# Kernel tuning notes

Measured on AMD Instinct MI355X. Metric: run time of the kernel, lower is better.

The kernel has to match this reference:

```python
import jax, jax.numpy as jnp
import numpy as np

SLOPE = 0.1  # supar MLP uses LeakyReLU(0.1)

def _mlp(x, W, b):
    return jax.nn.leaky_relu(x @ W + b, negative_slope=SLOPE)

def _triaffine(x, y, z, W):
    # supar Triaffine with n_out=1: s[b,z,x,y] = sum_{i,k,j} x[b,x,i] W[i,k,j] y[b,y,j] z[b,z,k]
    w = jnp.einsum('bzk,ikj->bzij', z, W)          # [b, n, d, d]
    return jnp.einsum('bxi,bzij,byj->bzxy', x, w, y)  # [b, n, n, n]

def _triu_sym(s):
    # s.triu() + s.triu(1).transpose(-1, -2) over last two dims
    return jnp.triu(s) + jnp.swapaxes(jnp.triu(s, 1), -1, -2)

def setup_inputs() -> dict:
    key = jax.random.key(0)
    B, N, D_IN, D = 2, 128, 1024, 150
    ks = jax.random.split(key, 16)
    sc_in = 1.0 / np.sqrt(D_IN)
    sc_tri = float(D) ** -1.5  # keeps triaffine outputs O(1)
    def nrm(k, shape, sc):
        return jax.random.normal(k, shape, jnp.float32) * sc
    return {
        'x':   jax.random.normal(ks[0], (B, N, D_IN), jnp.float32),
        'W_sh': nrm(ks[1], (D_IN, D), sc_in), 'b_sh': jnp.zeros((D,), jnp.float32),
        'W_st': nrm(ks[2], (D_IN, D), sc_in), 'b_st': jnp.zeros((D,), jnp.float32),
        'W_p':  nrm(ks[3], (D_IN, D), sc_in), 'b_p':  jnp.zeros((D,), jnp.float32),
        'T_pt':    nrm(ks[4], (D, D, D), sc_tri),
        'T_ph':    nrm(ks[5], (D, D, D), sc_tri),
        'T_phsib': nrm(ks[6], (D, D, D), sc_tri),
        'T_ptsib': nrm(ks[7], (D, D, D), sc_tri),
        'T_phcop': nrm(ks[8], (D, D, D), sc_tri),
        'T_ptcop': nrm(ks[9], (D, D, D), sc_tri),
    }

def reference(x, W_sh, b_sh, W_st, b_st, W_p, b_p,
              T_pt, T_ph, T_phsib, T_ptsib, T_phcop, T_ptcop):
    # eval mode: dropout is identity; ind_prd=False so p2 == p (shared MLP)
    sh = _mlp(x, W_sh, b_sh)
    st = _mlp(x, W_st, b_st)
    p = _mlp(x, W_p, b_p)
    p2 = p
    # span scores: [b, p, sh_idx, st_idx]
    span_pst = _triu_sym(_triaffine(sh, st, p2, T_pt))
    span_psh = _triaffine(sh, st, p, T_ph)
    # sibling scores: [b, p, h, h'] / [b, p, t, t']
    ph_sib = _triu_sym(_triaffine(sh, sh, p, T_phsib))
    pt_sib = _triu_sym(_triaffine(st, st, p2, T_ptsib))
    # co-parent scores: triaffine gives [b, h, p, p'], permute(0,2,3,1) -> [b, p, p', h]
    ph_cop = jnp.transpose(_triu_sym(_triaffine(p, p, sh, T_phcop)), (0, 2, 3, 1))
    pt_cop = jnp.transpose(_triu_sym(_triaffine(p2, p2, st, T_ptcop)), (0, 2, 3, 1))
    return (span_psh, span_pst, ph_sib, pt_sib, ph_cop, pt_cop)
```

## Files before the change

### kernel.cpp

```cpp
#include <hip/hip_runtime.h>


#define DD    150
#define KP    160
#define OUTBLK 4194304
#define NWZ   24064
#define TTG   3840000
#define WZG   (256*NWZ)
#define HROW  (256*160)

__device__ __forceinline__ unsigned short f2u(float f) {
  unsigned x = __float_as_uint(f);
  x += 0x7FFFu + ((x >> 16) & 1u);
  return (unsigned short)(x >> 16);
}

typedef __attribute__((ext_vector_type(8))) short frag8;
typedef __attribute__((ext_vector_type(4))) float facc4;
typedef __attribute__((ext_vector_type(4))) unsigned uint4v;

__constant__ int c_zsel[6] = {2, 2, 2, 2, 0, 1};
__constant__ int c_xsel[6] = {0, 0, 0, 1, 2, 2};
__constant__ int c_ysel[6] = {1, 1, 0, 1, 2, 2};

__global__ __launch_bounds__(256) void mlp_partial(
    const float* __restrict__ x,
    const float* __restrict__ W0, const float* __restrict__ W1, const float* __restrict__ W2,
    float* __restrict__ P)
{
  int m = blockIdx.x, bt = blockIdx.y, ks = blockIdx.z;
  const float* W = (m == 0) ? W0 : (m == 1) ? W1 : W2;
  int bn0 = bt * 32, k0 = ks * 128;
  __shared__ float xs[32][132];
  int tid = threadIdx.x;
  for (int e = 0; e < 4; ++e) {
    int l = e * 256 + tid;
    int row = l >> 5, c4 = l & 31;
    float4 v = *(const float4*)&x[(bn0 + row) * 1024 + k0 + c4 * 4];
    xs[row][c4 * 4 + 0] = v.x; xs[row][c4 * 4 + 1] = v.y;
    xs[row][c4 * 4 + 2] = v.z; xs[row][c4 * 4 + 3] = v.w;
  }
  __syncthreads();
  int tj = tid & 15, tt = tid >> 4, r = tt * 2;
  int dd[10];
  #pragma unroll
  for (int u = 0; u < 10; ++u) { int d = tj + 16 * u; dd[u] = d < 150 ? d : 149; }
  float a0[10], a1[10];
  #pragma unroll
  for (int u = 0; u < 10; ++u) { a0[u] = 0.f; a1[u] = 0.f; }
  for (int k = 0; k < 128; ++k) {
    float xa = xs[r][k], xb = xs[r + 1][k];
    const float* wr = W + (long long)(k0 + k) * 150;
    #pragma unroll
    for (int u = 0; u < 10; ++u) {
      float w = wr[dd[u]];
      a0[u] += xa * w; a1[u] += xb * w;
    }
  }
  float* Pb = P + (long long)(m * 8 + ks) * 256 * 160;
  #pragma unroll
  for (int u = 0; u < 10; ++u) {
    int d = tj + 16 * u;
    Pb[(bn0 + r) * 160 + d]     = a0[u];
    Pb[(bn0 + r + 1) * 160 + d] = a1[u];
  }
}

__global__ __launch_bounds__(256) void mlp_reduce(
    const float* __restrict__ P,
    const float* __restrict__ B0, const float* __restrict__ B1, const float* __restrict__ B2,
    unsigned short* __restrict__ H)
{
  int o = blockIdx.x * 256 + threadIdx.x;
  int d = o % 160;
  int bn = (o / 160) & 255;
  int m = o / (160 * 256);
  float v = 0.f;
  if (d < 150) {
    const float* Bv = (m == 0) ? B0 : (m == 1) ? B1 : B2;
    v = Bv[d];
    #pragma unroll
    for (int ks = 0; ks < 8; ++ks)
      v += P[((long long)(m * 8 + ks) * 256 + bn) * 160 + d];
    v = v > 0.f ? v : 0.1f * v;
  }
  H[o] = f2u(v);
}

struct TPtrs { const float* t[6]; };
__global__ __launch_bounds__(256) void tt_kernel(TPtrs tp, unsigned short* __restrict__ TT3)
{
  int i = blockIdx.x;
  int ky = blockIdx.y % 5, jy = blockIdx.y / 5;
  int k0 = ky * 32, j0 = jy * 32;
  int g = blockIdx.z;
  const float* T = tp.t[g];
  unsigned short* TT = TT3 + (long long)g * TTG;
  __shared__ float tl[32][33];
  int tid = threadIdx.x;
  #pragma unroll
  for (int e = 0; e < 4; ++e) {
    int l = e * 256 + tid;
    int r = l >> 5, c = l & 31;
    float v = 0.f;
    if (i < 150 && k0 + r < 150 && j0 + c < 150)
      v = T[i * 22500 + (k0 + r) * 150 + (j0 + c)];
    tl[r][c] = v;
  }
  __syncthreads();
  #pragma unroll
  for (int e = 0; e < 4; ++e) {
    int l = e * 256 + tid;
    int rr = l >> 5, cc = l & 31;
    if (j0 + rr < 150)
      TT[(long long)((j0 + rr) * 160 + i) * 160 + k0 + cc] = f2u(tl[cc][rr]);
  }
}

__global__ __launch_bounds__(256) void wz_gemm(
    const unsigned short* __restrict__ Hb, const unsigned short* __restrict__ TT3,
    unsigned short* __restrict__ wz3)
{
  constexpr int LR = 72;
  __shared__ unsigned short lA[128 * LR];
  __shared__ unsigned short lB[128 * LR];
  int g = blockIdx.z, tid = threadIdx.x;
  const unsigned short* Ab = Hb + c_zsel[g] * HROW + blockIdx.y * 128 * 160;
  const unsigned short* Bb = TT3 + (long long)g * TTG;
  int n0 = blockIdx.x * 128;
  int wave = tid >> 6, lane = tid & 63;
  int l15 = lane & 15, lq = lane >> 4;
  int mw = (wave & 1) * 64, nw = (wave >> 1) * 64;
  facc4 acc[4][4];
  #pragma unroll
  for (int i = 0; i < 4; ++i)
    #pragma unroll
    for (int j = 0; j < 4; ++j) acc[i][j] = (facc4){0.f, 0.f, 0.f, 0.f};
  for (int ch = 0; ch < 3; ++ch) {
    int k0 = ch << 6;
    int sh = (ch == 2) ? 2 : 3, upr = 1 << sh;
    for (int u = tid; u < 128 * upr; u += 256) {
      int row = u >> sh, off = (u & (upr - 1)) << 3;
      *(uint4*)&lA[row * LR + off] = *(const uint4*)&Ab[row * 160 + k0 + off];
    }
    for (int u = tid; u < 128 * upr; u += 256) {
      int row = u >> sh, off = (u & (upr - 1)) << 3;
      int gn = n0 + row;
      uint4 v; v.x = 0u; v.y = 0u; v.z = 0u; v.w = 0u;
      if (gn < 24000) v = *(const uint4*)&Bb[(long long)gn * 160 + k0 + off];
      *(uint4*)&lB[row * LR + off] = v;
    }
    __syncthreads();
    int nks = (ch == 2) ? 1 : 2;
    for (int ks = 0; ks < nks; ++ks) {
      int ko = (ks << 5) + (lq << 3);
      frag8 af[4], bfr[4];
      #pragma unroll
      for (int i = 0; i < 4; ++i) af[i] = *(const frag8*)&lA[(mw + i * 16 + l15) * LR + ko];
      #pragma unroll
      for (int j = 0; j < 4; ++j) bfr[j] = *(const frag8*)&lB[(nw + j * 16 + l15) * LR + ko];
      #pragma unroll
      for (int i = 0; i < 4; ++i)
        #pragma unroll
        for (int j = 0; j < 4; ++j)
          acc[i][j] = __builtin_amdgcn_mfma_f32_16x16x32_bf16(af[i], bfr[j], acc[i][j], 0, 0, 0);
    }
    __syncthreads();
  }
  unsigned short* C = wz3 + (long long)g * WZG;
  int mb = blockIdx.y * 128 + mw;
  #pragma unroll
  for (int i = 0; i < 4; ++i)
    #pragma unroll
    for (int r = 0; r < 4; ++r) {
      int m = mb + i * 16 + lq * 4 + r;
      #pragma unroll
      for (int j = 0; j < 4; ++j)
        C[(long long)m * NWZ + n0 + nw + j * 16 + l15] = f2u(acc[i][j][r]);
    }
}

struct SPtrs { float* p[6]; };
__global__ __launch_bounds__(256, 3) void tmps_gemm(
    const unsigned short* __restrict__ Hb, const unsigned short* __restrict__ wz3,
    SPtrs sp)
{
  __shared__ union {
    struct { unsigned short X[128 * 72]; unsigned short W[160 * 72]; } p1;
    unsigned short Y[128 * 168];
    float sq[64 * 129];
  } sm;

  int z = blockIdx.x, tid = threadIdx.x;
  int g = z >> 8, bz = z & 255, b = bz >> 7;
  const unsigned short* Ab = Hb + c_xsel[g] * HROW + b * 128 * 160;
  const unsigned short* Wb = wz3 + (long long)g * WZG + (long long)bz * NWZ;
  int wave = tid >> 6, lane = tid & 63;
  int l15 = lane & 15, lq = lane >> 4;
  int X0 = wave * 32;

  facc4 accT[10][2];
  #pragma unroll
  for (int jt = 0; jt < 10; ++jt)
    #pragma unroll
    for (int xt = 0; xt < 2; ++xt) accT[jt][xt] = (facc4){0.f, 0.f, 0.f, 0.f};
  for (int ch = 0; ch < 3; ++ch) {
    int k0 = ch << 6;
    int sh = (ch == 2) ? 2 : 3, upr = 1 << sh;
    for (int u = tid; u < 128 * upr; u += 256) {
      int row = u >> sh, off = (u & (upr - 1)) << 3;
      *(uint4*)&sm.p1.X[row * 72 + off] = *(const uint4*)&Ab[row * 160 + k0 + off];
    }
    for (int u = tid; u < 160 * upr; u += 256) {
      int row = u >> sh, off = (u & (upr - 1)) << 3;
      uint4 v; v.x = 0u; v.y = 0u; v.z = 0u; v.w = 0u;
      if (row < 150) v = *(const uint4*)&Wb[row * 160 + k0 + off];
      *(uint4*)&sm.p1.W[row * 72 + off] = v;
    }
    __syncthreads();
    int nks = (ch == 2) ? 1 : 2;
    for (int ks = 0; ks < nks; ++ks) {
      int ko = (ks << 5) + (lq << 3);
      frag8 bx0 = *(const frag8*)&sm.p1.X[(X0 + l15) * 72 + ko];
      frag8 bx1 = *(const frag8*)&sm.p1.X[(X0 + 16 + l15) * 72 + ko];
      #pragma unroll
      for (int jt = 0; jt < 10; ++jt) {
        frag8 aw = *(const frag8*)&sm.p1.W[(jt * 16 + l15) * 72 + ko];
        accT[jt][0] = __builtin_amdgcn_mfma_f32_16x16x32_bf16(aw, bx0, accT[jt][0], 0, 0, 0);
        accT[jt][1] = __builtin_amdgcn_mfma_f32_16x16x32_bf16(aw, bx1, accT[jt][1], 0, 0, 0);
      }
    }
    __syncthreads();
  }

  frag8 pA[2][5];
  {
    int s0 = ((lq & 1) << 5) + l15;
    int s2 = s0 + 16;
    bool lo = lq < 2;
    #pragma unroll
    for (int kb = 0; kb < 5; ++kb)
      #pragma unroll
      for (int xt = 0; xt < 2; ++xt) {
        unsigned w0l = (unsigned)f2u(accT[2 * kb][xt][0]) |
                       ((unsigned)f2u(accT[2 * kb][xt][1]) << 16);
        unsigned w1l = (unsigned)f2u(accT[2 * kb][xt][2]) |
                       ((unsigned)f2u(accT[2 * kb][xt][3]) << 16);
        unsigned w0h = (unsigned)f2u(accT[2 * kb + 1][xt][0]) |
                       ((unsigned)f2u(accT[2 * kb + 1][xt][1]) << 16);
        unsigned w1h = (unsigned)f2u(accT[2 * kb + 1][xt][2]) |
                       ((unsigned)f2u(accT[2 * kb + 1][xt][3]) << 16);
        unsigned a0 = __shfl(w0l, s0), b0 = __shfl(w0h, s0);
        unsigned a1 = __shfl(w1l, s0), b1 = __shfl(w1h, s0);
        unsigned a2 = __shfl(w0l, s2), b2 = __shfl(w0h, s2);
        unsigned a3 = __shfl(w1l, s2), b3 = __shfl(w1h, s2);
        uint4v uv;
        uv.x = lo ? a0 : b0;
        uv.y = lo ? a1 : b1;
        uv.z = lo ? a2 : b2;
        uv.w = lo ? a3 : b3;
        pA[xt][kb] = __builtin_bit_cast(frag8, uv);
      }
  }

  const unsigned short* Yb = Hb + c_ysel[g] * HROW + b * 128 * 160;
  {
    int y = tid & 127, part = tid >> 7;
    #pragma unroll
    for (int p = 0; p < 10; ++p) {
      int off = part * 80 + p * 8;
      *(uint4*)&sm.Y[y * 168 + off] = *(const uint4*)&Yb[y * 160 + off];
    }
  }
  __syncthreads();

  facc4 acc2[2][8];
  #pragma unroll
  for (int xt = 0; xt < 2; ++xt)
    #pragma unroll
    for (int yt = 0; yt < 8; ++yt) acc2[xt][yt] = (facc4){0.f, 0.f, 0.f, 0.f};
  #pragma unroll
  for (int ks = 0; ks < 5; ++ks) {
    int ko = (ks << 5) + (lq << 3);
    #pragma unroll
    for (int yt = 0; yt < 8; ++yt) {
      frag8 by = *(const frag8*)&sm.Y[(yt * 16 + l15) * 168 + ko];
      acc2[0][yt] = __builtin_amdgcn_mfma_f32_16x16x32_bf16(pA[0][ks], by, acc2[0][yt], 0, 0, 0);
      acc2[1][yt] = __builtin_amdgcn_mfma_f32_16x16x32_bf16(pA[1][ks], by, acc2[1][yt], 0, 0, 0);
    }
  }

  float* C = sp.p[g] + (long long)bz * 16384;
  if (g == 0) {
    #pragma unroll
    for (int xt = 0; xt < 2; ++xt)
      #pragma unroll
      for (int r = 0; r < 4; ++r) {
        int x = X0 + xt * 16 + lq * 4 + r;
        #pragma unroll
        for (int yt = 0; yt < 8; ++yt)
          C[x * 128 + yt * 16 + l15] = acc2[xt][yt][r];
      }
  } else if (g >= 4) {
    #pragma unroll
    for (int xt = 0; xt < 2; ++xt)
      #pragma unroll
      for (int r = 0; r < 4; ++r) {
        int x = X0 + xt * 16 + lq * 4 + r;
        #pragma unroll
        for (int yt = 0; yt < 8; ++yt) {
          int y = yt * 16 + l15;
          if (x <= y) C[x * 128 + y] = acc2[xt][yt][r];
        }
      }
  } else {
    #pragma unroll
    for (int xt = 0; xt < 2; ++xt)
      #pragma unroll
      for (int r = 0; r < 4; ++r) {
        int x = X0 + xt * 16 + lq * 4 + r;
        #pragma unroll
        for (int yt = 0; yt < 8; ++yt) {
          int y = yt * 16 + l15;
          if (y >= x) C[x * 128 + y] = acc2[xt][yt][r];
        }
      }
    __syncthreads();
    if (wave < 2) {
      #pragma unroll
      for (int xt = 0; xt < 2; ++xt)
        #pragma unroll
        for (int r = 0; r < 4; ++r) {
          int x = X0 + xt * 16 + lq * 4 + r;
          #pragma unroll
          for (int yt = 0; yt < 8; ++yt)
            sm.sq[x * 129 + yt * 16 + l15] = acc2[xt][yt][r];
        }
    }
    __syncthreads();
    for (int it = 0; it < 32; ++it) {
      int x = X0 + it;
      int y = lane;
      if (y < 64 && y < x) C[x * 128 + y] = sm.sq[y * 129 + x];
    }
    __syncthreads();
    if (wave >= 2) {
      #pragma unroll
      for (int xt = 0; xt < 2; ++xt)
        #pragma unroll
        for (int r = 0; r < 4; ++r) {
          int x = X0 + xt * 16 + lq * 4 + r;
          #pragma unroll
          for (int yt = 0; yt < 8; ++yt)
            sm.sq[(x - 64) * 129 + yt * 16 + l15] = acc2[xt][yt][r];
        }
    }
    __syncthreads();
    for (int it = 0; it < 16; ++it) {
      int x = 64 + wave * 16 + it;
      int y = 64 + lane;
      if (y < x) C[x * 128 + y] = sm.sq[(y - 64) * 129 + x];
    }
  }
}

__global__ __launch_bounds__(256) void cop_kernel(
    const float* __restrict__ ss, float* __restrict__ out)
{
  int w0 = blockIdx.x << 5;
  int z0 = blockIdx.y << 5;
  int g  = blockIdx.z >> 1, b = blockIdx.z & 1;
  const float* sg = ss + (long long)g * OUTBLK;
  float* outp = out + (long long)(4 + g) * OUTBLK;
  __shared__ float tl[32][33];
  int tid = threadIdx.x;
  #pragma unroll
  for (int e = 0; e < 4; ++e) {
    int l = e * 256 + tid;
    int r = l >> 5, c = l & 31;
    int w = w0 + c;
    int xx = w >> 7, yy = w & 127;
    int sx = xx < yy ? xx : yy;
    int sy = xx < yy ? yy : xx;
    tl[r][c] = sg[(((b << 7) + z0 + r) << 14) + (sx << 7) + sy];
  }
  __syncthreads();
  #pragma unroll
  for (int e = 0; e < 4; ++e) {
    int l = e * 256 + tid;
    int rr = l >> 5, cc = l & 31;
    outp[(b << 21) + ((w0 + rr) << 7) + z0 + cc] = tl[cc][rr];
  }
}

extern "C" void kernel_launch(void* const* d_in, const int* in_sizes, int n_in,
                              void* d_out, int out_size, void* d_ws, size_t ws_size,
                              hipStream_t stream)
{
  const float* x   = (const float*)d_in[0];
  const float* Wsh = (const float*)d_in[1];
  const float* bsh = (const float*)d_in[2];
  const float* Wst = (const float*)d_in[3];
  const float* bst = (const float*)d_in[4];
  const float* Wp  = (const float*)d_in[5];
  const float* bp  = (const float*)d_in[6];
  TPtrs tp;
  tp.t[0] = (const float*)d_in[8];
  tp.t[1] = (const float*)d_in[7];
  tp.t[2] = (const float*)d_in[9];
  tp.t[3] = (const float*)d_in[10];
  tp.t[4] = (const float*)d_in[11];
  tp.t[5] = (const float*)d_in[12];
  float* out = (float*)d_out;
  char* wsb = (char*)d_ws;

  unsigned short* Hb   = (unsigned short*)(wsb);
  unsigned short* TT3  = (unsigned short*)(wsb + 245760);
  unsigned short* wz3  = (unsigned short*)(wsb + 46325760);
  float* P  = (float*)wz3;
  float* ss = (float*)TT3;

  SPtrs sp;
  sp.p[0] = out + 0LL * OUTBLK;
  sp.p[1] = out + 1LL * OUTBLK;
  sp.p[2] = out + 2LL * OUTBLK;
  sp.p[3] = out + 3LL * OUTBLK;
  sp.p[4] = ss;
  sp.p[5] = ss + OUTBLK;

  mlp_partial<<<dim3(3, 8, 8),    256, 0, stream>>>(x, Wsh, Wst, Wp, P);
  mlp_reduce <<<dim3(480),        256, 0, stream>>>(P, bsh, bst, bp, Hb);
  tt_kernel  <<<dim3(160, 25, 6), 256, 0, stream>>>(tp, TT3);
  wz_gemm    <<<dim3(188, 2, 6),  256, 0, stream>>>(Hb, TT3, wz3);
  tmps_gemm  <<<dim3(1536),       256, 0, stream>>>(Hb, wz3, sp);
  cop_kernel <<<dim3(512, 4, 4),  256, 0, stream>>>(ss, out);
}
```

Measured before the change: 370.1 us.

## Stream X/Y fragments from global in tmps_gemm and move symmetrize to separate kernel

The tmps_gemm kernel stops staging the X and Y operands in shared memory and loads MFMA fragments directly from global memory, keeping only the W tile in LDS. The second GEMM is split into two halves to reduce accumulator registers, and the launch bound is raised to 4 blocks per CU. The in-kernel transpose-based lower-triangle fill for groups 1-3 is replaced by a new sym_fill kernel that mirrors the upper triangle using 32x32 shared-memory tiles. The aim is lower LDS use and fewer barriers for higher occupancy, at the cost of uncoalesced global fragment loads and an extra launch that rereads the outputs.

```diff
diff --git a/kernel.cpp b/kernel.cpp
--- a/kernel.cpp
+++ b/kernel.cpp
@@ -22,6 +22,8 @@
 __constant__ int c_zsel[6] = {2, 2, 2, 2, 0, 1};
 __constant__ int c_xsel[6] = {0, 0, 0, 1, 2, 2};
 __constant__ int c_ysel[6] = {1, 1, 0, 1, 2, 2};
+__constant__ int c_tx[10] = {0, 1, 1, 2, 2, 2, 3, 3, 3, 3};
+__constant__ int c_ty[10] = {0, 0, 1, 0, 1, 2, 0, 1, 2, 3};
 
 __global__ __launch_bounds__(256) void mlp_partial(
     const float* __restrict__ x,
@@ -181,15 +183,11 @@
 }
 
 struct SPtrs { float* p[6]; };
-__global__ __launch_bounds__(256, 3) void tmps_gemm(
+__global__ __launch_bounds__(256, 4) void tmps_gemm(
     const unsigned short* __restrict__ Hb, const unsigned short* __restrict__ wz3,
     SPtrs sp)
 {
-  __shared__ union {
-    struct { unsigned short X[128 * 72]; unsigned short W[160 * 72]; } p1;
-    unsigned short Y[128 * 168];
-    float sq[64 * 129];
-  } sm;
+  __shared__ unsigned short Wsm[160 * 72];
 
   int z = blockIdx.x, tid = threadIdx.x;
   int g = z >> 8, bz = z & 255, b = bz >> 7;
@@ -199,6 +197,9 @@
   int l15 = lane & 15, lq = lane >> 4;
   int X0 = wave * 32;
 
+  const unsigned short* Xr0 = Ab + (X0 + l15) * 160;
+  const unsigned short* Xr1 = Ab + (X0 + 16 + l15) * 160;
+
   facc4 accT[10][2];
   #pragma unroll
   for (int jt = 0; jt < 10; ++jt)
@@ -207,25 +208,21 @@
   for (int ch = 0; ch < 3; ++ch) {
     int k0 = ch << 6;
     int sh = (ch == 2) ? 2 : 3, upr = 1 << sh;
-    for (int u = tid; u < 128 * upr; u += 256) {
-      int row = u >> sh, off = (u & (upr - 1)) << 3;
-      *(uint4*)&sm.p1.X[row * 72 + off] = *(const uint4*)&Ab[row * 160 + k0 + off];
-    }
     for (int u = tid; u < 160 * upr; u += 256) {
       int row = u >> sh, off = (u & (upr - 1)) << 3;
       uint4 v; v.x = 0u; v.y = 0u; v.z = 0u; v.w = 0u;
       if (row < 150) v = *(const uint4*)&Wb[row * 160 + k0 + off];
-      *(uint4*)&sm.p1.W[row * 72 + off] = v;
+      *(uint4*)&Wsm[row * 72 + off] = v;
     }
     __syncthreads();
     int nks = (ch == 2) ? 1 : 2;
     for (int ks = 0; ks < nks; ++ks) {
       int ko = (ks << 5) + (lq << 3);
-      frag8 bx0 = *(const frag8*)&sm.p1.X[(X0 + l15) * 72 + ko];
-      frag8 bx1 = *(const frag8*)&sm.p1.X[(X0 + 16 + l15) * 72 + ko];
+      frag8 bx0 = *(const frag8*)&Xr0[k0 + ko];
+      frag8 bx1 = *(const frag8*)&Xr1[k0 + ko];
       #pragma unroll
       for (int jt = 0; jt < 10; ++jt) {
-        frag8 aw = *(const frag8*)&sm.p1.W[(jt * 16 + l15) * 72 + ko];
+        frag8 aw = *(const frag8*)&Wsm[(jt * 16 + l15) * 72 + ko];
         accT[jt][0] = __builtin_amdgcn_mfma_f32_16x16x32_bf16(aw, bx0, accT[jt][0], 0, 0, 0);
         accT[jt][1] = __builtin_amdgcn_mfma_f32_16x16x32_bf16(aw, bx1, accT[jt][1], 0, 0, 0);
       }
@@ -264,103 +261,59 @@
   }
 
   const unsigned short* Yb = Hb + c_ysel[g] * HROW + b * 128 * 160;
-  {
-    int y = tid & 127, part = tid >> 7;
-    #pragma unroll
-    for (int p = 0; p < 10; ++p) {
-      int off = part * 80 + p * 8;
-      *(uint4*)&sm.Y[y * 168 + off] = *(const uint4*)&Yb[y * 160 + off];
-    }
-  }
-  __syncthreads();
-
-  facc4 acc2[2][8];
-  #pragma unroll
-  for (int xt = 0; xt < 2; ++xt)
-    #pragma unroll
-    for (int yt = 0; yt < 8; ++yt) acc2[xt][yt] = (facc4){0.f, 0.f, 0.f, 0.f};
-  #pragma unroll
-  for (int ks = 0; ks < 5; ++ks) {
-    int ko = (ks << 5) + (lq << 3);
-    #pragma unroll
-    for (int yt = 0; yt < 8; ++yt) {
-      frag8 by = *(const frag8*)&sm.Y[(yt * 16 + l15) * 168 + ko];
-      acc2[0][yt] = __builtin_amdgcn_mfma_f32_16x16x32_bf16(pA[0][ks], by, acc2[0][yt], 0, 0, 0);
-      acc2[1][yt] = __builtin_amdgcn_mfma_f32_16x16x32_bf16(pA[1][ks], by, acc2[1][yt], 0, 0, 0);
-    }
-  }
-
   float* C = sp.p[g] + (long long)bz * 16384;
-  if (g == 0) {
+  for (int h = 0; h < 2; ++h) {
+    facc4 acc2[2][4];
+    #pragma unroll
+    for (int xt = 0; xt < 2; ++xt)
+      #pragma unroll
+      for (int j = 0; j < 4; ++j) acc2[xt][j] = (facc4){0.f, 0.f, 0.f, 0.f};
+    #pragma unroll
+    for (int ks = 0; ks < 5; ++ks) {
+      int ko = (ks << 5) + (lq << 3);
+      #pragma unroll
+      for (int j = 0; j < 4; ++j) {
+        frag8 by = *(const frag8*)&Yb[((h * 4 + j) * 16 + l15) * 160 + ko];
+        acc2[0][j] = __builtin_amdgcn_mfma_f32_16x16x32_bf16(pA[0][ks], by, acc2[0][j], 0, 0, 0);
+        acc2[1][j] = __builtin_amdgcn_mfma_f32_16x16x32_bf16(pA[1][ks], by, acc2[1][j], 0, 0, 0);
+      }
+    }
     #pragma unroll
     for (int xt = 0; xt < 2; ++xt)
       #pragma unroll
       for (int r = 0; r < 4; ++r) {
         int x = X0 + xt * 16 + lq * 4 + r;
         #pragma unroll
-        for (int yt = 0; yt < 8; ++yt)
-          C[x * 128 + yt * 16 + l15] = acc2[xt][yt][r];
-      }
-  } else if (g >= 4) {
-    #pragma unroll
-    for (int xt = 0; xt < 2; ++xt)
-      #pragma unroll
-      for (int r = 0; r < 4; ++r) {
-        int x = X0 + xt * 16 + lq * 4 + r;
-        #pragma unroll
-        for (int yt = 0; yt < 8; ++yt) {
-          int y = yt * 16 + l15;
-          if (x <= y) C[x * 128 + y] = acc2[xt][yt][r];
+        for (int j = 0; j < 4; ++j) {
+          int y = (h * 4 + j) * 16 + l15;
+          if (g == 0 || x <= y) C[x * 128 + y] = acc2[xt][j][r];
         }
       }
-  } else {
-    #pragma unroll
-    for (int xt = 0; xt < 2; ++xt)
-      #pragma unroll
-      for (int r = 0; r < 4; ++r) {
-        int x = X0 + xt * 16 + lq * 4 + r;
-        #pragma unroll
-        for (int yt = 0; yt < 8; ++yt) {
-          int y = yt * 16 + l15;
-          if (y >= x) C[x * 128 + y] = acc2[xt][yt][r];
-        }
-      }
-    __syncthreads();
-    if (wave < 2) {
-      #pragma unroll
-      for (int xt = 0; xt < 2; ++xt)
-        #pragma unroll
-        for (int r = 0; r < 4; ++r) {
-          int x = X0 + xt * 16 + lq * 4 + r;
-          #pragma unroll
-          for (int yt = 0; yt < 8; ++yt)
-            sm.sq[x * 129 + yt * 16 + l15] = acc2[xt][yt][r];
-        }
-    }
-    __syncthreads();
-    for (int it = 0; it < 32; ++it) {
-      int x = X0 + it;
-      int y = lane;
-      if (y < 64 && y < x) C[x * 128 + y] = sm.sq[y * 129 + x];
-    }
-    __syncthreads();
-    if (wave >= 2) {
-      #pragma unroll
-      for (int xt = 0; xt < 2; ++xt)
-        #pragma unroll
-        for (int r = 0; r < 4; ++r) {
-          int x = X0 + xt * 16 + lq * 4 + r;
-          #pragma unroll
-          for (int yt = 0; yt < 8; ++yt)
-            sm.sq[(x - 64) * 129 + yt * 16 + l15] = acc2[xt][yt][r];
-        }
-    }
-    __syncthreads();
-    for (int it = 0; it < 16; ++it) {
-      int x = 64 + wave * 16 + it;
-      int y = 64 + lane;
-      if (y < x) C[x * 128 + y] = sm.sq[(y - 64) * 129 + x];
-    }
+  }
+}
+
+__global__ __launch_bounds__(256) void sym_fill(float* __restrict__ out)
+{
+  int zb = blockIdx.x;
+  int grp = zb >> 8, bz = zb & 255;
+  int t = blockIdx.y;
+  int x0 = c_tx[t] << 5, y0 = c_ty[t] << 5;
+  float* S = out + (long long)(1 + grp) * OUTBLK + (long long)bz * 16384;
+  __shared__ float tl[32][33];
+  int tid = threadIdx.x;
+  #pragma unroll
+  for (int e = 0; e < 4; ++e) {
+    int l = e * 256 + tid;
+    int r = l >> 5, c = l & 31;
+    tl[r][c] = S[(y0 + r) * 128 + x0 + c];
+  }
+  __syncthreads();
+  #pragma unroll
+  for (int e = 0; e < 4; ++e) {
+    int l = e * 256 + tid;
+    int rr = l >> 5, cc = l & 31;
+    int x = x0 + rr, y = y0 + cc;
+    if (x > y) S[x * 128 + y] = tl[cc][rr];
   }
 }
 
@@ -433,5 +386,6 @@
   tt_kernel  <<<dim3(160, 25, 6), 256, 0, stream>>>(tp, TT3);
   wz_gemm    <<<dim3(188, 2, 6),  256, 0, stream>>>(Hb, TT3, wz3);
   tmps_gemm  <<<dim3(1536),       256, 0, stream>>>(Hb, wz3, sp);
+  sym_fill   <<<dim3(768, 10),    256, 0, stream>>>(out);
   cop_kernel <<<dim3(512, 4, 4),  256, 0, stream>>>(ss, out);
 }
```

New measurement: 365.3 us. Within noise of the previous version (-1.3%).
